# Kernel tuning notes

Measured on AMD Instinct MI355X. Metric: run time of the kernel, lower is better.

The kernel has to match this reference:

```python
import jax, jax.numpy as jnp
import numpy as np
from jax import lax

N_NODES = 50000
N_EDGES = 800000
IN_DIM = 256
H_DIM = 128     # per-head out_dim
N_HEADS = 2
HID = H_DIM * N_HEADS  # 256
OUT_DIM = 256
NEG_SLOPE = 0.2


def setup_inputs() -> dict:
    key = jax.random.key(0)
    ks = jax.random.split(key, 20)
    s = 0.05
    inp = {}
    inp["in_feat"] = jax.random.normal(ks[0], (N_NODES, IN_DIM), jnp.float32)
    inp["src"] = jax.random.randint(ks[1], (N_EDGES,), 0, N_NODES, jnp.int32)
    inp["dst"] = jax.random.randint(ks[2], (N_EDGES,), 0, N_NODES, jnp.int32)
    # GAT layer 1 (heads stacked on leading axis)
    inp["W1"]  = jax.random.normal(ks[3], (N_HEADS, H_DIM, IN_DIM), jnp.float32) * s
    inp["as1"] = jax.random.normal(ks[4], (N_HEADS, H_DIM), jnp.float32) * s
    inp["ad1"] = jax.random.normal(ks[5], (N_HEADS, H_DIM), jnp.float32) * s
    # GAT layer 2 (input dim = HID)
    inp["W2"]  = jax.random.normal(ks[6], (N_HEADS, H_DIM, HID), jnp.float32) * s
    inp["as2"] = jax.random.normal(ks[7], (N_HEADS, H_DIM), jnp.float32) * s
    inp["ad2"] = jax.random.normal(ks[8], (N_HEADS, H_DIM), jnp.float32) * s
    # Bidirectional GRU over the L=2 layer outputs (input=hidden=HID)
    inp["wi_f"] = jax.random.normal(ks[9],  (3 * HID, HID), jnp.float32) * s
    inp["wh_f"] = jax.random.normal(ks[10], (3 * HID, HID), jnp.float32) * s
    inp["bi_f"] = jax.random.normal(ks[11], (3 * HID,), jnp.float32) * s
    inp["bh_f"] = jax.random.normal(ks[12], (3 * HID,), jnp.float32) * s
    inp["wi_b"] = jax.random.normal(ks[13], (3 * HID, HID), jnp.float32) * s
    inp["wh_b"] = jax.random.normal(ks[14], (3 * HID, HID), jnp.float32) * s
    inp["bi_b"] = jax.random.normal(ks[15], (3 * HID,), jnp.float32) * s
    inp["bh_b"] = jax.random.normal(ks[16], (3 * HID,), jnp.float32) * s
    # JKN attention + output linear
    inp["s_w"]   = jax.random.normal(ks[17], (2 * HID,), jnp.float32) * s
    inp["lin_w"] = jax.random.normal(ks[18], (OUT_DIM, 2 * HID), jnp.float32) * s
    return inp


def _gat(x, W, a_s, a_d, src, dst):
    """Multi-head GAT: per-dst edge-softmax, scatter-sum aggregation."""
    N = x.shape[0]
    z = jnp.einsum('nd,hod->hno', x, W)           # [H,N,O]
    es = jnp.einsum('hno,ho->hn', z, a_s)          # [H,N]
    ed = jnp.einsum('hno,ho->hn', z, a_d)          # [H,N]
    e = jax.nn.leaky_relu(es[:, src] + ed[:, dst], NEG_SLOPE)  # [H,E]

    def per_head(e_h, z_h):
        m = jnp.full((N,), -jnp.inf, e_h.dtype).at[dst].max(e_h)   # segment max
        ex = jnp.exp(e_h - m[dst])
        den = jax.ops.segment_sum(ex, dst, num_segments=N)
        a = ex / den[dst]                                          # edge softmax
        return jax.ops.segment_sum(a[:, None] * z_h[src], dst, num_segments=N)

    outs = jax.vmap(per_head)(e, z)                # [H,N,O]
    return jnp.transpose(outs, (1, 0, 2)).reshape(N, -1)  # head concat [N,H*O]


def _gru_dir(xs, Wi, Wh, bi, bh, reverse):
    """PyTorch-style GRU over leading (layer) axis. xs: [L,N,D]."""
    H = Wh.shape[1]

    def step(h, x):
        gi = x @ Wi.T + bi
        gh = h @ Wh.T + bh
        ir, iz, inn = jnp.split(gi, 3, axis=-1)
        hr, hz, hn = jnp.split(gh, 3, axis=-1)
        r = jax.nn.sigmoid(ir + hr)
        zt = jax.nn.sigmoid(iz + hz)
        n = jnp.tanh(inn + r * hn)
        h_new = (1.0 - zt) * n + zt * h
        return h_new, h_new

    h0 = jnp.zeros((xs.shape[1], H), xs.dtype)
    _, ys = lax.scan(step, h0, xs, reverse=reverse)
    return ys  # [L,N,H]


def reference(in_feat, src, dst, W1, as1, ad1, W2, as2, ad2,
              wi_f, wh_f, bi_f, bh_f, wi_b, wh_b, bi_b, bh_b, s_w, lin_w):
    h1 = jax.nn.relu(_gat(in_feat, W1, as1, ad1, src, dst))   # [N,HID]
    h2 = jax.nn.relu(_gat(h1, W2, as2, ad2, src, dst))        # [N,HID]
    hs = jnp.stack([h1, h2], axis=0)                          # [L=2,N,HID]
    f = _gru_dir(hs, wi_f, wh_f, bi_f, bh_f, False)
    b = _gru_dir(hs, wi_b, wh_b, bi_b, bh_b, True)
    h_seq = jnp.concatenate([f, b], axis=-1)                  # [L,N,2*HID]
    # Faithful to source: softmax over last dim of [L,N,1] (identically 1.0)
    w = jax.nn.softmax((h_seq @ s_w)[..., None], axis=-1)     # [L,N,1]
    h_N = jnp.einsum('lni,lnf->nf', w, h_seq)                 # [N,2*HID]
    return h_N @ lin_w.T                                      # [N,OUT_DIM]
```

## Files before the change

kernel.cpp:

```cpp
#include <hip/hip_runtime.h>
#include <hip/hip_bf16.h>

#define NN 50000
#define NE 800000
#define MP 50048
#define NBLK 196

typedef __attribute__((ext_vector_type(8))) short short8;
typedef __attribute__((ext_vector_type(4))) float f32x4;

__device__ __forceinline__ float b2f(__hip_bfloat16 x) { return __bfloat162float(x); }
__device__ __forceinline__ __hip_bfloat16 f2b(float x) { return __float2bfloat16(x); }
__device__ __forceinline__ float bu2f(unsigned short u) { return __uint_as_float(((unsigned)u) << 16); }
__device__ __forceinline__ unsigned short f2bu(float x) { __hip_bfloat16 b = f2b(x); return *(unsigned short*)&b; }
__device__ __forceinline__ float sigm(float x) { return 1.f / (1.f + __expf(-x)); }
__device__ __forceinline__ float leaky(float x) { return x >= 0.f ? x : 0.2f * x; }

__device__ __forceinline__ void gload16(const void* g, void* l) {
  __builtin_amdgcn_global_load_lds((__attribute__((address_space(1))) void*)(g),
                                   (__attribute__((address_space(3))) void*)(l), 16, 0, 0);
}

__global__ void diag_kernel(float* out, float v) { out[0] = v; }

__global__ void zero_i32(int* p, int n) {
  int i = blockIdx.x * 256 + threadIdx.x;
  if (i < n) p[i] = 0;
}

__global__ void conv_kernel(const float* __restrict__ in, __hip_bfloat16* __restrict__ out, int n) {
  for (int i = blockIdx.x * blockDim.x + threadIdx.x; i < n; i += gridDim.x * blockDim.x)
    out[i] = f2b(in[i]);
}

__global__ void conv4_kernel(const float* __restrict__ in, __hip_bfloat16* __restrict__ out, int n4) {
  int i = blockIdx.x * 256 + threadIdx.x;
  if (i >= n4) return;
  float4 v = ((const float4*)in)[i];
  ushort4 o;
  o.x = f2bu(v.x); o.y = f2bu(v.y); o.z = f2bu(v.z); o.w = f2bu(v.w);
  ((ushort4*)out)[i] = o;
}

__global__ void conv_gruw(const float* __restrict__ p0, const float* __restrict__ p1,
                          const float* __restrict__ p2, const float* __restrict__ p3,
                          __hip_bfloat16* __restrict__ out) {
  int idx = blockIdx.x * 256 + threadIdx.x;
  int w = idx / 196608, r = idx - w * 196608;
  const float* s = (w == 0) ? p0 : (w == 1) ? p1 : (w == 2) ? p2 : p3;
  out[idx] = f2b(s[r]);
}

__global__ void conv_strided(const float* __restrict__ in, __hip_bfloat16* __restrict__ out,
                             int rows, int cols, int ld, int coff) {
  int idx = blockIdx.x * 256 + threadIdx.x;
  if (idx >= rows * cols) return;
  int r = idx / cols, c = idx - r * cols;
  out[idx] = f2b(in[(size_t)r * ld + coff + c]);
}

#define EPI_ESED 0
#define EPI_OUT  1

template <int EPI, bool DUAL>
__global__ __launch_bounds__(256, 2) void gemmF(
    const __hip_bfloat16* __restrict__ A1, const __hip_bfloat16* __restrict__ B1,
    const __hip_bfloat16* __restrict__ A2, const __hip_bfloat16* __restrict__ B2,
    void* __restrict__ Cv, int M, int N,
    const float* __restrict__ bi, const float* __restrict__ bh,
    float* __restrict__ ESp, float* __restrict__ EDp) {
  __shared__ __align__(16) short smem[32768];
  const int tid = threadIdx.x;
  const int wid = tid >> 6, lane = tid & 63;

  const int NW = gridDim.x * gridDim.y;
  const int wg = blockIdx.x + gridDim.x * blockIdx.y;
  const int q = NW >> 3, r8 = NW & 7;
  const int xcd = wg & 7, jj = wg >> 3;
  const int wid2 = (xcd < r8 ? xcd * (q + 1) : r8 * (q + 1) + (xcd - r8) * q) + jj;
  const int m0 = (wid2 / gridDim.x) * 128, n0 = (wid2 % gridDim.x) * 128;

  const int NPH = DUAL ? 4 : 2;
  f32x4 acc[2][8];
#pragma unroll
  for (int rf = 0; rf < 2; ++rf)
#pragma unroll
    for (int cf = 0; cf < 8; ++cf) acc[rf][cf] = (f32x4)0.f;

  for (int p = 0; p < NPH; ++p) {
    const __hip_bfloat16* A = (DUAL && p >= 2) ? A2 : A1;
    const __hip_bfloat16* B = (DUAL && p >= 2) ? B2 : B1;
    const int k0 = (p & 1) * 128;
#pragma unroll
    for (int i = 0; i < 8; ++i) {
      int qi = wid * 8 + i;
      int rl = qi * 4 + (lane >> 4);
      int sl = (lane & 15) ^ (rl & 15);
      gload16(A + (size_t)(m0 + rl) * 256 + k0 + sl * 8, &smem[qi * 512]);
      gload16(B + (size_t)(n0 + rl) * 256 + k0 + sl * 8, &smem[16384 + qi * 512]);
    }
    asm volatile("s_waitcnt vmcnt(0)" ::: "memory");
    __builtin_amdgcn_s_barrier();
    __builtin_amdgcn_sched_barrier(0);
#pragma unroll
    for (int kc = 0; kc < 4; ++kc) {
      const int sl = ((kc * 4 + (lane >> 4)) ^ (lane & 15)) * 8;
      short8 af[2];
#pragma unroll
      for (int rf = 0; rf < 2; ++rf)
        af[rf] = *(const short8*)&smem[(wid * 32 + rf * 16 + (lane & 15)) * 128 + sl];
#pragma unroll
      for (int cf = 0; cf < 8; ++cf) {
        short8 bf = *(const short8*)&smem[16384 + (cf * 16 + (lane & 15)) * 128 + sl];
#pragma unroll
        for (int rf = 0; rf < 2; ++rf)
          acc[rf][cf] = __builtin_amdgcn_mfma_f32_16x16x32_bf16(af[rf], bf, acc[rf][cf], 0, 0, 0);
      }
    }
    asm volatile("s_waitcnt lgkmcnt(0)" ::: "memory");
    __builtin_amdgcn_sched_barrier(0);
    __builtin_amdgcn_s_barrier();
  }

  const int rowb = m0 + wid * 32 + (lane >> 4) * 4;
  const int colb = n0 + (lane & 15);

  if constexpr (EPI == EPI_ESED) {
    const int head = n0 >> 7;
#pragma unroll
    for (int rf = 0; rf < 2; ++rf) {
#pragma unroll
      for (int rr = 0; rr < 4; ++rr) {
        const int row = rowb + rf * 16 + rr;
        float ps = 0.f, pd = 0.f;
#pragma unroll
        for (int cf = 0; cf < 8; ++cf) {
          const int col = colb + cf * 16;
          float v = acc[rf][cf][rr];
          if (row < M) ((__hip_bfloat16*)Cv)[(size_t)row * N + col] = f2b(v);
          ps += v * bi[col];
          pd += v * bh[col];
        }
#pragma unroll
        for (int o = 8; o >= 1; o >>= 1) {
          ps += __shfl_xor(ps, o, 64);
          pd += __shfl_xor(pd, o, 64);
        }
        if ((lane & 15) == 0 && row < M) {
          ESp[row * 2 + head] = ps;
          EDp[row * 2 + head] = pd;
        }
      }
    }
    return;
  }
#pragma unroll
  for (int rf = 0; rf < 2; ++rf)
#pragma unroll
    for (int cf = 0; cf < 8; ++cf) {
      const int col = colb + cf * 16;
#pragma unroll
      for (int rr = 0; rr < 4; ++rr) {
        const int row = rowb + rf * 16 + rr;
        if (row < M) ((float*)Cv)[(size_t)row * 256 + col] = acc[rf][cf][rr];
      }
    }
}

template <int STEP>
__global__ __launch_bounds__(256) void gruF(
    const __hip_bfloat16* __restrict__ hF, const __hip_bfloat16* __restrict__ WiF,
    const __hip_bfloat16* __restrict__ hpF, const __hip_bfloat16* __restrict__ WhF,
    const float* __restrict__ biF, const float* __restrict__ bhF,
    __hip_bfloat16* __restrict__ outF,
    const __hip_bfloat16* __restrict__ hB, const __hip_bfloat16* __restrict__ WiB,
    const __hip_bfloat16* __restrict__ hpB, const __hip_bfloat16* __restrict__ WhB,
    const float* __restrict__ biB, const float* __restrict__ bhB,
    __hip_bfloat16* __restrict__ outB) {
  __shared__ __align__(16) short smem[14336];
  const int tid = threadIdx.x;
  const int wid = tid >> 6, lane = tid & 63;

  const int NW = gridDim.x * gridDim.y;
  const int wg = blockIdx.x + gridDim.x * blockIdx.y;
  const int q = NW >> 3, r8 = NW & 7;
  const int xcd = wg & 7, jj = wg >> 3;
  const int wid2 = (xcd < r8 ? xcd * (q + 1) : r8 * (q + 1) + (xcd - r8) * q) + jj;
  const int bx2 = wid2 & 15;
  const int m0 = (wid2 >> 4) * 128;
  const int dir = bx2 >> 3;
  const int nc0 = (bx2 & 7) * 32;

  const __hip_bfloat16* Ah = dir ? hB : hF;
  const __hip_bfloat16* Wi = dir ? WiB : WiF;
  const __hip_bfloat16* Ahp = dir ? hpB : hpF;
  const __hip_bfloat16* Wh = dir ? WhB : WhF;
  const float* bi = dir ? biB : biF;
  const float* bh = dir ? bhB : bhF;
  __hip_bfloat16* outp = dir ? outB : outF;

  f32x4 acc[2][6];
  f32x4 accNh[2][2];
#pragma unroll
  for (int rf = 0; rf < 2; ++rf) {
#pragma unroll
    for (int j = 0; j < 6; ++j) acc[rf][j] = (f32x4)0.f;
#pragma unroll
    for (int j = 0; j < 2; ++j) accNh[rf][j] = (f32x4)0.f;
  }

  auto stage = [&](const __hip_bfloat16* A, const __hip_bfloat16* W, int k0) {
#pragma unroll
    for (int i = 0; i < 4; ++i) {
      int qi = wid * 4 + i;
      int rl = qi * 8 + (lane >> 3);
      int sl = (lane & 7) ^ (rl & 7);
      gload16(A + (size_t)(m0 + rl) * 256 + k0 + sl * 8, &smem[qi * 512]);
    }
#pragma unroll
    for (int i = 0; i < 3; ++i) {
      int qi = wid * 3 + i;
      int rl = qi * 8 + (lane >> 3);
      int wrow = (rl >> 5) * 256 + nc0 + (rl & 31);
      int sl = (lane & 7) ^ (rl & 7);
      gload16(W + (size_t)wrow * 256 + k0 + sl * 8, &smem[8192 + qi * 512]);
    }
  };

  auto computeP = [&](auto PASSC) {
    constexpr int PASS = decltype(PASSC)::value;
#pragma unroll
    for (int kc = 0; kc < 2; ++kc) {
      short8 af[2];
#pragma unroll
      for (int rf = 0; rf < 2; ++rf) {
        const int arow = wid * 32 + rf * 16 + (lane & 15);
        const int pa = ((kc * 4 + (lane >> 4)) ^ (arow & 7)) * 8;
        af[rf] = *(const short8*)&smem[arow * 64 + pa];
      }
#pragma unroll
      for (int j = 0; j < 6; ++j) {
        const int brow = j * 16 + (lane & 15);
        const int pb = ((kc * 4 + (lane >> 4)) ^ (brow & 7)) * 8;
        short8 bf = *(const short8*)&smem[8192 + brow * 64 + pb];
#pragma unroll
        for (int rf = 0; rf < 2; ++rf) {
          if constexpr (PASS == 1) {
            if (j >= 4)
              accNh[rf][j - 4] = __builtin_amdgcn_mfma_f32_16x16x32_bf16(af[rf], bf, accNh[rf][j - 4], 0, 0, 0);
            else
              acc[rf][j] = __builtin_amdgcn_mfma_f32_16x16x32_bf16(af[rf], bf, acc[rf][j], 0, 0, 0);
          } else {
            acc[rf][j] = __builtin_amdgcn_mfma_f32_16x16x32_bf16(af[rf], bf, acc[rf][j], 0, 0, 0);
          }
        }
      }
    }
  };

  const int NPH = (STEP == 1) ? 4 : 8;
  for (int p = 0; p < NPH; ++p) {
    const int k0 = (p & 3) * 64;
    if (STEP == 2 && p >= 4) stage(Ahp, Wh, k0);
    else stage(Ah, Wi, k0);
    asm volatile("s_waitcnt vmcnt(0)" ::: "memory");
    __builtin_amdgcn_s_barrier();
    __builtin_amdgcn_sched_barrier(0);
    if (STEP == 2 && p >= 4) computeP(std::integral_constant<int, 1>{});
    else computeP(std::integral_constant<int, 0>{});
    asm volatile("s_waitcnt lgkmcnt(0)" ::: "memory");
    __builtin_amdgcn_sched_barrier(0);
    __builtin_amdgcn_s_barrier();
  }

#pragma unroll
  for (int cf = 0; cf < 2; ++cf) {
    const int col = nc0 + cf * 16 + (lane & 15);
    const float brz = bi[col] + bh[col];
    const float bzz = bi[256 + col] + bh[256 + col];
    const float bin = bi[512 + col];
    const float bhn = bh[512 + col];
#pragma unroll
    for (int rf = 0; rf < 2; ++rf) {
#pragma unroll
      for (int rr = 0; rr < 4; ++rr) {
        const int row = m0 + wid * 32 + rf * 16 + (lane >> 4) * 4 + rr;
        if (row >= NN) continue;
        float r_ = sigm(acc[rf][cf][rr] + brz);
        float z_ = sigm(acc[rf][2 + cf][rr] + bzz);
        if constexpr (STEP == 1) {
          float n_ = tanhf(acc[rf][4 + cf][rr] + bin + r_ * bhn);
          outp[(size_t)row * 256 + col] = f2b((1.f - z_) * n_);
        } else {
          float n_ = tanhf(acc[rf][4 + cf][rr] + bin + r_ * (accNh[rf][cf][rr] + bhn));
          float hp = b2f(Ahp[(size_t)row * 256 + col]);
          outp[(size_t)row * 256 + col] = f2b(hp + (1.f - z_) * n_ + z_ * hp);
        }
      }
    }
  }
}

__global__ void hist_kernel(const int* __restrict__ dst, int* __restrict__ deg, int ne) {
  for (int e = blockIdx.x * blockDim.x + threadIdx.x; e < ne; e += gridDim.x * blockDim.x)
    atomicAdd(&deg[dst[e]], 1);
}

__global__ void scan1(const int* __restrict__ deg, int* __restrict__ bsum, int n) {
  __shared__ int sd[256];
  int idx = blockIdx.x * 256 + threadIdx.x;
  sd[threadIdx.x] = (idx < n) ? deg[idx] : 0;
  __syncthreads();
  for (int off = 128; off > 0; off >>= 1) {
    if (threadIdx.x < off) sd[threadIdx.x] += sd[threadIdx.x + off];
    __syncthreads();
  }
  if (threadIdx.x == 0) bsum[blockIdx.x] = sd[0];
}

__global__ void scan2(const int* __restrict__ bsum, int* __restrict__ boff, int nb) {
  __shared__ int s[256];
  int t = threadIdx.x;
  int v0 = (t < nb) ? bsum[t] : 0;
  s[t] = v0;
  __syncthreads();
  for (int off = 1; off < 256; off <<= 1) {
    int x = (t >= off) ? s[t - off] : 0;
    __syncthreads();
    s[t] += x;
    __syncthreads();
  }
  if (t < nb) boff[t] = s[t] - v0;
}

__global__ void scan3(const int* __restrict__ deg, const int* __restrict__ boff,
                      int* __restrict__ row_ptr, int* __restrict__ cursor, int n, int ne) {
  __shared__ int s[256];
  int t = threadIdx.x;
  int idx = blockIdx.x * 256 + t;
  int v = (idx < n) ? deg[idx] : 0;
  s[t] = v;
  __syncthreads();
  for (int off = 1; off < 256; off <<= 1) {
    int x = (t >= off) ? s[t - off] : 0;
    __syncthreads();
    s[t] += x;
    __syncthreads();
  }
  if (idx < n) {
    int val = boff[blockIdx.x] + s[t] - v;
    row_ptr[idx] = val;
    cursor[idx] = val;
  }
  if (idx == n) row_ptr[n] = ne;
}

__global__ void scatter_kernel(const int* __restrict__ src, const int* __restrict__ dst,
                               int* __restrict__ cursor, int* __restrict__ srcs, int ne) {
  for (int e = blockIdx.x * blockDim.x + threadIdx.x; e < ne; e += gridDim.x * blockDim.x) {
    int p = atomicAdd(&cursor[dst[e]], 1);
    srcs[p] = src[e];
  }
}

__device__ __forceinline__ void onl_upd(float& m, float& s, float v) {
  if (v <= m) {
    s += __expf(v - m);
  } else {
    s = s * __expf(m - v) + 1.f;
    m = v;
  }
}

__global__ __launch_bounds__(256) void gat_agg_wave(const int* __restrict__ row_ptr,
                                                    const int* __restrict__ srcs,
                                                    const float* __restrict__ es,
                                                    const float* __restrict__ ed,
                                                    const __hip_bfloat16* __restrict__ z,
                                                    __hip_bfloat16* __restrict__ hout) {
  int node = blockIdx.x * 4 + (threadIdx.x >> 6);
  int lane = threadIdx.x & 63;
  if (node >= NN) return;
  ushort4* outp = (ushort4*)&hout[(size_t)node * 256 + lane * 4];
  int start = row_ptr[node], end = row_ptr[node + 1];
  int deg = end - start;
  if (deg == 0) {
    *outp = make_ushort4(0, 0, 0, 0);
    return;
  }
  float ed0 = ed[node * 2], ed1 = ed[node * 2 + 1];
  int h = lane >> 5;
  float a0 = 0.f, a1 = 0.f, a2 = 0.f, a3 = 0.f;

  if (deg <= 64) {
    int sn = 0;
    float l0 = -1e30f, l1 = -1e30f;
    if (lane < deg) {
      sn = srcs[start + lane];
      float2 ee = *(const float2*)&es[sn * 2];
      l0 = leaky(ee.x + ed0);
      l1 = leaky(ee.y + ed1);
    }
    float m0 = l0, m1 = l1;
#pragma unroll
    for (int off = 32; off > 0; off >>= 1) {
      m0 = fmaxf(m0, __shfl_xor(m0, off, 64));
      m1 = fmaxf(m1, __shfl_xor(m1, off, 64));
    }
    float p0 = (lane < deg) ? __expf(l0 - m0) : 0.f;
    float p1 = (lane < deg) ? __expf(l1 - m1) : 0.f;
    float s0 = p0, s1 = p1;
#pragma unroll
    for (int off = 32; off > 0; off >>= 1) {
      s0 += __shfl_xor(s0, off, 64);
      s1 += __shfl_xor(s1, off, 64);
    }
    float w0 = p0 / s0, w1 = p1 / s1;
    const size_t zlo = lane * 4;
    int e = 0;
    for (; e + 4 <= deg; e += 4) {
      int sa = __shfl(sn, e, 64), sb = __shfl(sn, e + 1, 64);
      int sc = __shfl(sn, e + 2, 64), sd = __shfl(sn, e + 3, 64);
      float wa0 = __shfl(w0, e, 64),     wa1 = __shfl(w1, e, 64);
      float wb0 = __shfl(w0, e + 1, 64), wb1 = __shfl(w1, e + 1, 64);
      float wc0 = __shfl(w0, e + 2, 64), wc1 = __shfl(w1, e + 2, 64);
      float wd0 = __shfl(w0, e + 3, 64), wd1 = __shfl(w1, e + 3, 64);
      float wa = h ? wa1 : wa0;
      float wb = h ? wb1 : wb0;
      float wc = h ? wc1 : wc0;
      float wd = h ? wd1 : wd0;
      ushort4 za = *(const ushort4*)&z[(size_t)sa * 256 + zlo];
      ushort4 zb = *(const ushort4*)&z[(size_t)sb * 256 + zlo];
      ushort4 zc = *(const ushort4*)&z[(size_t)sc * 256 + zlo];
      ushort4 zd = *(const ushort4*)&z[(size_t)sd * 256 + zlo];
      a0 = fmaf(wa, bu2f(za.x), a0); a1 = fmaf(wa, bu2f(za.y), a1);
      a2 = fmaf(wa, bu2f(za.z), a2); a3 = fmaf(wa, bu2f(za.w), a3);
      a0 = fmaf(wb, bu2f(zb.x), a0); a1 = fmaf(wb, bu2f(zb.y), a1);
      a2 = fmaf(wb, bu2f(zb.z), a2); a3 = fmaf(wb, bu2f(zb.w), a3);
      a0 = fmaf(wc, bu2f(zc.x), a0); a1 = fmaf(wc, bu2f(zc.y), a1);
      a2 = fmaf(wc, bu2f(zc.z), a2); a3 = fmaf(wc, bu2f(zc.w), a3);
      a0 = fmaf(wd, bu2f(zd.x), a0); a1 = fmaf(wd, bu2f(zd.y), a1);
      a2 = fmaf(wd, bu2f(zd.z), a2); a3 = fmaf(wd, bu2f(zd.w), a3);
    }
    for (; e < deg; ++e) {
      int sa = __shfl(sn, e, 64);
      float wa0 = __shfl(w0, e, 64), wa1 = __shfl(w1, e, 64);
      float wa = h ? wa1 : wa0;
      ushort4 za = *(const ushort4*)&z[(size_t)sa * 256 + zlo];
      a0 = fmaf(wa, bu2f(za.x), a0); a1 = fmaf(wa, bu2f(za.y), a1);
      a2 = fmaf(wa, bu2f(za.z), a2); a3 = fmaf(wa, bu2f(za.w), a3);
    }
  } else {
    float m0 = -1e30f, s0 = 0.f, m1 = -1e30f, s1 = 0.f;
    for (int i = start + lane; i < end; i += 64) {
      int sn = srcs[i];
      float e0 = es[sn * 2], e1 = es[sn * 2 + 1];
      onl_upd(m0, s0, leaky(e0 + ed0));
      onl_upd(m1, s1, leaky(e1 + ed1));
    }
#pragma unroll
    for (int off = 32; off > 0; off >>= 1) {
      float om0 = __shfl_xor(m0, off, 64), os0 = __shfl_xor(s0, off, 64);
      float om1 = __shfl_xor(m1, off, 64), os1 = __shfl_xor(s1, off, 64);
      float mm = fmaxf(m0, om0);
      s0 = s0 * __expf(m0 - mm) + os0 * __expf(om0 - mm);
      m0 = mm;
      mm = fmaxf(m1, om1);
      s1 = s1 * __expf(m1 - mm) + os1 * __expf(om1 - mm);
      m1 = mm;
    }
    float rm = h ? m1 : m0;
    float rsi = 1.f / (h ? s1 : s0);
    float edh = h ? ed1 : ed0;
    for (int e = start; e < end; ++e) {
      int sa = srcs[e];
      float2 ee = *(const float2*)&es[sa * 2];
      float w = __expf(leaky((h ? ee.y : ee.x) + edh) - rm) * rsi;
      ushort4 zv = *(const ushort4*)&z[(size_t)sa * 256 + lane * 4];
      a0 = fmaf(w, bu2f(zv.x), a0); a1 = fmaf(w, bu2f(zv.y), a1);
      a2 = fmaf(w, bu2f(zv.z), a2); a3 = fmaf(w, bu2f(zv.w), a3);
    }
  }
  ushort4 o;
  o.x = f2bu(fmaxf(a0, 0.f));
  o.y = f2bu(fmaxf(a1, 0.f));
  o.z = f2bu(fmaxf(a2, 0.f));
  o.w = f2bu(fmaxf(a3, 0.f));
  *outp = o;
}

extern "C" void kernel_launch(void* const* d_in, const int* in_sizes, int n_in,
                              void* d_out, int out_size, void* d_ws, size_t ws_size,
                              hipStream_t stream) {
  const float* in_feat = (const float*)d_in[0];
  const int* srcp = (const int*)d_in[1];
  const int* dstp = (const int*)d_in[2];
  const float* W1 = (const float*)d_in[3];
  const float* as1 = (const float*)d_in[4];
  const float* ad1 = (const float*)d_in[5];
  const float* W2 = (const float*)d_in[6];
  const float* as2 = (const float*)d_in[7];
  const float* ad2 = (const float*)d_in[8];
  const float* wi_f = (const float*)d_in[9];
  const float* wh_f = (const float*)d_in[10];
  const float* bi_f = (const float*)d_in[11];
  const float* bh_f = (const float*)d_in[12];
  const float* wi_b = (const float*)d_in[13];
  const float* wh_b = (const float*)d_in[14];
  const float* bi_b = (const float*)d_in[15];
  const float* bh_b = (const float*)d_in[16];
  const float* lin_w = (const float*)d_in[18];
  (void)in_sizes; (void)n_in; (void)out_size;

  const size_t UNIT = (size_t)MP * 256 * 2;
  char* ws = (char*)d_ws;
  size_t off = 0;
  auto take = [&](size_t bytes) -> void* {
    void* p = ws + off;
    off += (bytes + 255) & ~(size_t)255;
    return p;
  };
  __hip_bfloat16* U0 = (__hip_bfloat16*)take(UNIT);
  __hip_bfloat16* U1 = (__hip_bfloat16*)take(UNIT * 2);
  __hip_bfloat16* h1 = (__hip_bfloat16*)take(UNIT);
  __hip_bfloat16* h2 = (__hip_bfloat16*)take(UNIT);
  __hip_bfloat16* hpF = (__hip_bfloat16*)take(UNIT);
  __hip_bfloat16* hpB = (__hip_bfloat16*)take(UNIT);
  __hip_bfloat16* wW1 = (__hip_bfloat16*)take(65536 * 2);
  __hip_bfloat16* wW2 = (__hip_bfloat16*)take(65536 * 2);
  __hip_bfloat16* wif = (__hip_bfloat16*)take(196608 * 2);
  __hip_bfloat16* whf = (__hip_bfloat16*)take(196608 * 2);
  __hip_bfloat16* wib = (__hip_bfloat16*)take(196608 * 2);
  __hip_bfloat16* whb = (__hip_bfloat16*)take(196608 * 2);
  __hip_bfloat16* wlinA = (__hip_bfloat16*)take(65536 * 2);
  __hip_bfloat16* wlinB = (__hip_bfloat16*)take(65536 * 2);
  int* deg = (int*)take((size_t)NN * 4);
  float* es1 = (float*)take((size_t)NN * 2 * 4);
  float* ed1 = (float*)take((size_t)NN * 2 * 4);
  float* es2 = (float*)take((size_t)NN * 2 * 4);
  float* ed2 = (float*)take((size_t)NN * 2 * 4);
  int* cursor = (int*)take((size_t)NN * 4);
  int* row_ptr = (int*)take((size_t)(NN + 1) * 4);
  int* bsum = (int*)take(256 * 4);
  int* boff = (int*)take(256 * 4);
  int* srcs = (int*)take((size_t)NE * 4);

  if (off > ws_size) {
    diag_kernel<<<1, 1, 0, stream>>>((float*)d_out, (float)ws_size);
    return;
  }

  conv4_kernel<<<12500, 256, 0, stream>>>(in_feat, U0, NN * 64);
  conv_kernel<<<256, 256, 0, stream>>>(W1, wW1, 65536);
  conv_kernel<<<256, 256, 0, stream>>>(W2, wW2, 65536);
  conv_gruw<<<3072, 256, 0, stream>>>(wi_f, wh_f, wi_b, wh_b, wif);
  conv_strided<<<256, 256, 0, stream>>>(lin_w, wlinA, 256, 256, 512, 0);
  conv_strided<<<256, 256, 0, stream>>>(lin_w, wlinB, 256, 256, 512, 256);

  {
    int zw = (int)(((char*)ed2 - (char*)deg) / 4) + NN * 2;
    zero_i32<<<(zw + 255) / 256, 256, 0, stream>>>(deg, zw);
  }
  hist_kernel<<<1024, 256, 0, stream>>>(dstp, deg, NE);
  scan1<<<NBLK, 256, 0, stream>>>(deg, bsum, NN);
  scan2<<<1, 256, 0, stream>>>(bsum, boff, NBLK);
  scan3<<<NBLK, 256, 0, stream>>>(deg, boff, row_ptr, cursor, NN, NE);
  scatter_kernel<<<1024, 256, 0, stream>>>(srcp, dstp, cursor, srcs, NE);

  dim3 g2(2, MP / 128), gGRU(16, MP / 128);

  gemmF<EPI_ESED, false><<<g2, 256, 0, stream>>>(U0, wW1, nullptr, nullptr, U1, NN, 256,
                                                 as1, ad1, es1, ed1);
  gat_agg_wave<<<12500, 256, 0, stream>>>(row_ptr, srcs, es1, ed1, U1, h1);
  gemmF<EPI_ESED, false><<<g2, 256, 0, stream>>>(h1, wW2, nullptr, nullptr, U1, NN, 256,
                                                 as2, ad2, es2, ed2);
  gat_agg_wave<<<12500, 256, 0, stream>>>(row_ptr, srcs, es2, ed2, U1, h2);

  gruF<1><<<gGRU, 256, 0, stream>>>(
      h1, wif, nullptr, nullptr, bi_f, bh_f, hpF,
      h2, wib, nullptr, nullptr, bi_b, bh_b, hpB);
  gruF<2><<<gGRU, 256, 0, stream>>>(
      h2, wif, hpF, whf, bi_f, bh_f, U0,
      h1, wib, hpB, whb, bi_b, bh_b, U1);

  gemmF<EPI_OUT, true><<<g2, 256, 0, stream>>>(U0, wlinA, U1, wlinB, d_out, NN, 256,
                                               nullptr, nullptr, nullptr, nullptr);
}
```

Measured before the change: 502.9 us.

## Prefetch GRU GEMM tiles via registers and shrink gemmF LDS tile for occupancy

gemmF now stages 64-wide K slices instead of 128 and uses half the shared memory, with an 8-way XOR swizzle and twice as many phases. The launch_bounds minimum-blocks hint is dropped, so occupancy may rise. The GRU kernel drops direct global-to-LDS loads and prefetches the next K-slice into registers while the current slice is computed, then writes it to LDS. This overlaps global latency with MFMA work at the cost of more registers and extra barriers.

```diff
diff --git a/kernel.cpp b/kernel.cpp
--- a/kernel.cpp
+++ b/kernel.cpp
@@ -63,13 +63,13 @@
 #define EPI_OUT  1
 
 template <int EPI, bool DUAL>
-__global__ __launch_bounds__(256, 2) void gemmF(
+__global__ __launch_bounds__(256) void gemmF(
     const __hip_bfloat16* __restrict__ A1, const __hip_bfloat16* __restrict__ B1,
     const __hip_bfloat16* __restrict__ A2, const __hip_bfloat16* __restrict__ B2,
     void* __restrict__ Cv, int M, int N,
     const float* __restrict__ bi, const float* __restrict__ bh,
     float* __restrict__ ESp, float* __restrict__ EDp) {
-  __shared__ __align__(16) short smem[32768];
+  __shared__ __align__(16) short smem[16384];
   const int tid = threadIdx.x;
   const int wid = tid >> 6, lane = tid & 63;
 
@@ -80,7 +80,7 @@
   const int wid2 = (xcd < r8 ? xcd * (q + 1) : r8 * (q + 1) + (xcd - r8) * q) + jj;
   const int m0 = (wid2 / gridDim.x) * 128, n0 = (wid2 % gridDim.x) * 128;
 
-  const int NPH = DUAL ? 4 : 2;
+  const int NPH = DUAL ? 8 : 4;
   f32x4 acc[2][8];
 #pragma unroll
   for (int rf = 0; rf < 2; ++rf)
@@ -88,30 +88,34 @@
     for (int cf = 0; cf < 8; ++cf) acc[rf][cf] = (f32x4)0.f;
 
   for (int p = 0; p < NPH; ++p) {
-    const __hip_bfloat16* A = (DUAL && p >= 2) ? A2 : A1;
-    const __hip_bfloat16* B = (DUAL && p >= 2) ? B2 : B1;
-    const int k0 = (p & 1) * 128;
-#pragma unroll
-    for (int i = 0; i < 8; ++i) {
-      int qi = wid * 8 + i;
-      int rl = qi * 4 + (lane >> 4);
-      int sl = (lane & 15) ^ (rl & 15);
+    const __hip_bfloat16* A = (DUAL && p >= 4) ? A2 : A1;
+    const __hip_bfloat16* B = (DUAL && p >= 4) ? B2 : B1;
+    const int k0 = (p & 3) * 64;
+#pragma unroll
+    for (int i = 0; i < 4; ++i) {
+      int qi = wid * 4 + i;
+      int rl = qi * 8 + (lane >> 3);
+      int sl = (lane & 7) ^ (rl & 7);
       gload16(A + (size_t)(m0 + rl) * 256 + k0 + sl * 8, &smem[qi * 512]);
-      gload16(B + (size_t)(n0 + rl) * 256 + k0 + sl * 8, &smem[16384 + qi * 512]);
+      gload16(B + (size_t)(n0 + rl) * 256 + k0 + sl * 8, &smem[8192 + qi * 512]);
     }
     asm volatile("s_waitcnt vmcnt(0)" ::: "memory");
     __builtin_amdgcn_s_barrier();
     __builtin_amdgcn_sched_barrier(0);
 #pragma unroll
-    for (int kc = 0; kc < 4; ++kc) {
-      const int sl = ((kc * 4 + (lane >> 4)) ^ (lane & 15)) * 8;
+    for (int kc = 0; kc < 2; ++kc) {
       short8 af[2];
 #pragma unroll
-      for (int rf = 0; rf < 2; ++rf)
-        af[rf] = *(const short8*)&smem[(wid * 32 + rf * 16 + (lane & 15)) * 128 + sl];
+      for (int rf = 0; rf < 2; ++rf) {
+        const int arow = wid * 32 + rf * 16 + (lane & 15);
+        const int pa = ((kc * 4 + (lane >> 4)) ^ (arow & 7)) * 8;
+        af[rf] = *(const short8*)&smem[arow * 64 + pa];
+      }
 #pragma unroll
       for (int cf = 0; cf < 8; ++cf) {
-        short8 bf = *(const short8*)&smem[16384 + (cf * 16 + (lane & 15)) * 128 + sl];
+        const int brow = cf * 16 + (lane & 15);
+        const int pb = ((kc * 4 + (lane >> 4)) ^ (brow & 7)) * 8;
+        short8 bf = *(const short8*)&smem[8192 + brow * 64 + pb];
 #pragma unroll
         for (int rf = 0; rf < 2; ++rf)
           acc[rf][cf] = __builtin_amdgcn_mfma_f32_16x16x32_bf16(af[rf], bf, acc[rf][cf], 0, 0, 0);
@@ -209,13 +213,14 @@
     for (int j = 0; j < 2; ++j) accNh[rf][j] = (f32x4)0.f;
   }
 
-  auto stage = [&](const __hip_bfloat16* A, const __hip_bfloat16* W, int k0) {
+  float4 rA[4], rW[3];
+  auto loadRegs = [&](const __hip_bfloat16* A, const __hip_bfloat16* W, int k0) {
 #pragma unroll
     for (int i = 0; i < 4; ++i) {
       int qi = wid * 4 + i;
       int rl = qi * 8 + (lane >> 3);
       int sl = (lane & 7) ^ (rl & 7);
-      gload16(A + (size_t)(m0 + rl) * 256 + k0 + sl * 8, &smem[qi * 512]);
+      rA[i] = *(const float4*)(A + (size_t)(m0 + rl) * 256 + k0 + sl * 8);
     }
 #pragma unroll
     for (int i = 0; i < 3; ++i) {
@@ -223,8 +228,16 @@
       int rl = qi * 8 + (lane >> 3);
       int wrow = (rl >> 5) * 256 + nc0 + (rl & 31);
       int sl = (lane & 7) ^ (rl & 7);
-      gload16(W + (size_t)wrow * 256 + k0 + sl * 8, &smem[8192 + qi * 512]);
-    }
+      rW[i] = *(const float4*)(W + (size_t)wrow * 256 + k0 + sl * 8);
+    }
+  };
+  auto writeLDS = [&]() {
+#pragma unroll
+    for (int i = 0; i < 4; ++i)
+      *(float4*)&smem[(wid * 4 + i) * 512 + lane * 8] = rA[i];
+#pragma unroll
+    for (int i = 0; i < 3; ++i)
+      *(float4*)&smem[8192 + (wid * 3 + i) * 512 + lane * 8] = rW[i];
   };
 
   auto computeP = [&](auto PASSC) {
@@ -259,18 +272,22 @@
   };
 
   const int NPH = (STEP == 1) ? 4 : 8;
+  loadRegs(Ah, Wi, 0);
+  writeLDS();
+  __syncthreads();
   for (int p = 0; p < NPH; ++p) {
-    const int k0 = (p & 3) * 64;
-    if (STEP == 2 && p >= 4) stage(Ahp, Wh, k0);
-    else stage(Ah, Wi, k0);
-    asm volatile("s_waitcnt vmcnt(0)" ::: "memory");
-    __builtin_amdgcn_s_barrier();
-    __builtin_amdgcn_sched_barrier(0);
+    if (p + 1 < NPH) {
+      const int k0n = ((p + 1) & 3) * 64;
+      if (STEP == 2 && p + 1 >= 4) loadRegs(Ahp, Wh, k0n);
+      else loadRegs(Ah, Wi, k0n);
+    }
     if (STEP == 2 && p >= 4) computeP(std::integral_constant<int, 1>{});
     else computeP(std::integral_constant<int, 0>{});
-    asm volatile("s_waitcnt lgkmcnt(0)" ::: "memory");
-    __builtin_amdgcn_sched_barrier(0);
-    __builtin_amdgcn_s_barrier();
+    __syncthreads();
+    if (p + 1 < NPH) {
+      writeLDS();
+      __syncthreads();
+    }
   }
 
 #pragma unroll
```

Result: slower. 1.007 ms (+100.1%).
